# Kernel optimization log

Measured on AMD Instinct MI355X. Metric: run time of the kernel, lower is better.

## Reference

```python
import jax, jax.numpy as jnp
import numpy as np

WIN_SIZE = 9
SIGMA = 1.5
K1, K2 = 0.01, 0.03
ALPHA, BETA = 0.5, 1.0
DATA_RANGE = 2.0
COV_NORM = 1.0  # use_sample_covariance=False


def _gaussian_window():
    coords = jnp.arange(WIN_SIZE, dtype=jnp.float32) - WIN_SIZE // 2
    g = jnp.exp(-coords ** 2 / (2.0 * SIGMA ** 2))
    g = g / g.sum()
    w2d = jnp.outer(g, g)  # [9, 9]
    return w2d[None, None, :, :]  # [1, 1, 9, 9] (OIHW, in_channel=1)


def setup_inputs() -> dict:
    key = jax.random.key(0)
    k1, k2 = jax.random.split(key)
    shape = (32, 1, 1024, 1024)
    X = jax.random.uniform(k1, shape, dtype=jnp.float32) * 2.0 - 1.0
    Y = jax.random.uniform(k2, shape, dtype=jnp.float32) * 2.0 - 1.0
    w = _gaussian_window()
    return {"X": X, "Y": Y, "w": w}


def _dwconv(x, w):
    # depthwise (groups=1 here since in_channel=1), VALID padding (use_pad=False)
    return jax.lax.conv_general_dilated(
        x, w, window_strides=(1, 1), padding="VALID",
        dimension_numbers=("NCHW", "OIHW", "NCHW"), feature_group_count=1)


def reference(X, Y, w):
    C1 = (K1 * DATA_RANGE) ** 2
    C2 = (K2 * DATA_RANGE) ** 2
    ux = _dwconv(X, w)
    uy = _dwconv(Y, w)
    uxx = _dwconv(X * X, w)
    uyy = _dwconv(Y * Y, w)
    uxy = _dwconv(X * Y, w)
    vx = COV_NORM * (uxx - ux * ux)
    vy = COV_NORM * (uyy - uy * uy)
    vxy = COV_NORM * (uxy - ux * uy)
    A1 = 2.0 * ux * uy + C1
    A2 = 2.0 * vxy + C2
    B1 = ux ** 2 + uy ** 2 + C1
    B2 = vx + vy + C2
    S = (A1 * A2) / (B1 * B2)
    ssim_loss = (1.0 - S).mean()
    loss_l1 = jnp.abs(X - Y).mean()
    return ALPHA * ssim_loss + BETA * loss_l1
```

## Files before the change

### kernel.cpp

```cpp
#include <hip/hip_runtime.h>

#define NT 256
#define RROWS 45
#define STRIP 256
#define PW 264
#define NLD 132
#define WID 1024
#define HEI 1024
#define OWD 1016

typedef float v2f __attribute__((ext_vector_type(2)));

template<int I> struct IC { static constexpr int v = I; };
template<int N, int I = 0, typename F>
__device__ __forceinline__ void sfor(F&& f) {
    if constexpr (I < N) { f(IC<I>{}); sfor<N, I + 1>(f); }
}

static __device__ __forceinline__ v2f pkfma(v2f a, v2f b, v2f c) {
#if __has_builtin(__builtin_elementwise_fma)
    return __builtin_elementwise_fma(a, b, c);
#else
    v2f r; r.x = fmaf(a.x, b.x, c.x); r.y = fmaf(a.y, b.y, c.y); return r;
#endif
}

__global__ __launch_bounds__(NT, 2)
void ssim_main(const float* __restrict__ X, const float* __restrict__ Y,
               const float* __restrict__ Wg, double* __restrict__ acc)
{
    __shared__ float2 Prow[9][PW];
    __shared__ float  wsum[4][2];

    const int t  = threadIdx.x;
    const int r0 = blockIdx.x * RROWS;
    const int c0 = blockIdx.y * STRIP;
    const size_t ibase = (size_t)blockIdx.z * (size_t)(WID * HEI);

    const bool ldv  = (t < NLD) && (c0 + 2 * t < WID);
    const bool ownc = (t < 128);

    float g[9];
    {
        float s = 0.f;
        sfor<9>([&](auto K) { constexpr int k = decltype(K)::v;
            g[k] = Wg[36 + k]; s += g[k]; });
        float rs = __builtin_amdgcn_rcpf(s);
        sfor<9>([&](auto K) { constexpr int k = decltype(K)::v; g[k] *= rs; });
    }

    const float C1 = 0.0004f, C2 = 0.0036f;
    float ssim_acc = 0.f, l1_acc = 0.f;

    v2f  r01[9], r23[9];
    float r4[9];
    float2 pbx[3], pby[3];

    const float2* __restrict__ Xp = (const float2*)(X + ibase + c0);
    const float2* __restrict__ Yp = (const float2*)(Y + ibase + c0);

    auto issue = [&](int ro, auto S) {
        constexpr int s = decltype(S)::v;
        const int row = r0 + ro;
        if (ldv && row < HEI) {
            pbx[s] = Xp[(size_t)row * (WID / 2) + t];
            pby[s] = Yp[(size_t)row * (WID / 2) + t];
        }
    };
    auto store = [&](int ro, auto S, auto LS) {
        constexpr int s  = decltype(S)::v;
        constexpr int ls = decltype(LS)::v;
        const int row = r0 + ro;
        if (ldv && row < HEI) {
            float4* dst = (float4*)&Prow[ls][2 * t];
            *dst = make_float4(pbx[s].x, pby[s].x, pbx[s].y, pby[s].y);
            if (ownc && ro < RROWS)
                l1_acc += fabsf(pbx[s].x - pby[s].x) + fabsf(pbx[s].y - pby[s].y);
        }
    };
    auto hcomp = [&](auto LS, auto RS) {
        constexpr int ls = decltype(LS)::v;
        constexpr int rs = decltype(RS)::v;
        v2f s01 = (v2f)0.f, s23 = (v2f)0.f; float s4 = 0.f;
        sfor<9>([&](auto K) { constexpr int k = decltype(K)::v;
            float2 p = Prow[ls][t + k];
            v2f a = { p.x, p.y };
            v2f gk2 = { g[k], g[k] };
            s01 = pkfma(gk2, a, s01);
            s23 = pkfma(gk2, a * a, s23);
            s4  = fmaf(g[k], p.x * p.y, s4);
        });
        r01[rs] = s01; r23[rs] = s23; r4[rs] = s4;
    };

    const bool vA = (c0 + t < OWD);

    auto outrow = [&](int j, auto JM) {
        constexpr int jm = decltype(JM)::v;
        if (r0 + j < OWD) {
            v2f u01 = (v2f)0.f, u23 = (v2f)0.f; float u4 = 0.f;
            sfor<9>([&](auto K) { constexpr int k = decltype(K)::v;
                constexpr int s = (jm + k) % 9;
                v2f gk2 = { g[k], g[k] };
                u01 = pkfma(gk2, r01[s], u01);
                u23 = pkfma(gk2, r23[s], u23);
                u4  = fmaf(g[k], r4[s], u4);
            });
            float ux = u01.x, uy = u01.y, uxx = u23.x, uyy = u23.y, uxy = u4;
            float uxux = ux * ux, uyuy = uy * uy, uxuy = ux * uy;
            float A1 = 2.f * uxuy + C1;
            float A2 = 2.f * (uxy - uxuy) + C2;
            float B1 = uxux + uyuy + C1;
            float B2 = (uxx - uxux) + (uyy - uyuy) + C2;
            float S  = (A1 * A2) * __builtin_amdgcn_rcpf(B1 * B2);
            ssim_acc += vA ? S : 0.f;
        }
    };

    issue(0, IC<0>{}); issue(1, IC<1>{}); issue(2, IC<2>{});
    store(0, IC<0>{}, IC<0>{}); store(1, IC<1>{}, IC<1>{}); store(2, IC<2>{}, IC<2>{});
    __syncthreads();
    issue(3, IC<0>{}); issue(4, IC<1>{}); issue(5, IC<2>{});
    hcomp(IC<0>{}, IC<0>{}); hcomp(IC<1>{}, IC<1>{}); hcomp(IC<2>{}, IC<2>{});

    store(3, IC<0>{}, IC<3>{}); store(4, IC<1>{}, IC<4>{}); store(5, IC<2>{}, IC<5>{});
    __syncthreads();
    issue(6, IC<0>{}); issue(7, IC<1>{}); issue(8, IC<2>{});
    hcomp(IC<3>{}, IC<3>{}); hcomp(IC<4>{}, IC<4>{}); hcomp(IC<5>{}, IC<5>{});

    store(6, IC<0>{}, IC<6>{}); store(7, IC<1>{}, IC<7>{}); store(8, IC<2>{}, IC<8>{});
    __syncthreads();
    issue(9, IC<0>{}); issue(10, IC<1>{}); issue(11, IC<2>{});
    hcomp(IC<6>{}, IC<6>{}); hcomp(IC<7>{}, IC<7>{});

#pragma unroll 1
    for (int P = 0; P < 5; ++P) {
        const int jb = 9 * P;
        sfor<3>([&](auto Q) {
            constexpr int q = decltype(Q)::v;
            const int p  = 3 * P + q;
            const int j0 = jb + 3 * q;
            store(j0 + 9,  IC<0>{}, IC<(3 * q) % 9>{});
            store(j0 + 10, IC<1>{}, IC<(3 * q + 1) % 9>{});
            store(j0 + 11, IC<2>{}, IC<(3 * q + 2) % 9>{});
            __syncthreads();
            if (p < 14) {
                issue(j0 + 12, IC<0>{}); issue(j0 + 13, IC<1>{}); issue(j0 + 14, IC<2>{});
            }
            hcomp(IC<(3 * q + 8) % 9>{}, IC<(3 * q + 8) % 9>{});
            outrow(j0,     IC<(3 * q) % 9>{});
            hcomp(IC<(3 * q + 9) % 9>{}, IC<(3 * q + 9) % 9>{});
            outrow(j0 + 1, IC<(3 * q + 1) % 9>{});
            hcomp(IC<(3 * q + 10) % 9>{}, IC<(3 * q + 10) % 9>{});
            outrow(j0 + 2, IC<(3 * q + 2) % 9>{});
        });
    }

#pragma unroll
    for (int off = 32; off > 0; off >>= 1) {
        ssim_acc += __shfl_down(ssim_acc, off);
        l1_acc   += __shfl_down(l1_acc, off);
    }
    const int wid = t >> 6;
    if ((t & 63) == 0) { wsum[wid][0] = ssim_acc; wsum[wid][1] = l1_acc; }
    __syncthreads();
    if (t == 0) {
        double s = 0.0, l = 0.0;
#pragma unroll
        for (int w = 0; w < 4; ++w) { s += (double)wsum[w][0]; l += (double)wsum[w][1]; }
        atomicAdd(acc + 0, s);
        atomicAdd(acc + 1, l);
    }
}

__global__ void ssim_final(const double* __restrict__ acc, float* __restrict__ out)
{
    const double n_ssim = 33032192.0;
    const double n_l1   = 33554432.0;
    double ssim_loss = 1.0 - acc[0] / n_ssim;
    double l1        = acc[1] / n_l1;
    out[0] = (float)(0.5 * ssim_loss + 1.0 * l1);
}

extern "C" void kernel_launch(void* const* d_in, const int* in_sizes, int n_in,
                              void* d_out, int out_size, void* d_ws, size_t ws_size,
                              hipStream_t stream)
{
    const float* X  = (const float*)d_in[0];
    const float* Y  = (const float*)d_in[1];
    const float* Wg = (const float*)d_in[2];
    float*  out = (float*)d_out;
    double* acc = (double*)d_ws;

    hipMemsetAsync(acc, 0, 2 * sizeof(double), stream);
    dim3 grid(23, 4, 32);
    ssim_main<<<grid, NT, 0, stream>>>(X, Y, Wg, acc);
    ssim_final<<<1, 1, 0, stream>>>(acc, out);
}
```

Measured before the change: 318.6 us.

## Stream rows into LDS ring via direct global_load_lds DMA

Replaces the register-staged loads and interleaved LDS stores with direct global-to-LDS loads (global_load_lds) into a 12-slot ring of separate X and Y row buffers. Synchronisation moves to manual vmcnt waits plus s_barrier, which keeps loads several rows ahead. The L1 term is now read back from LDS instead of registers. The aim is to cut VGPR staging and store instructions and to deepen the prefetch. The risk is fragile vmcnt accounting, tail-row handling and extra LDS space.

```diff
diff --git a/kernel.cpp b/kernel.cpp
--- a/kernel.cpp
+++ b/kernel.cpp
@@ -3,8 +3,8 @@
 #define NT 256
 #define RROWS 45
 #define STRIP 256
-#define PW 264
-#define NLD 132
+#define PWL 264
+#define NRING 12
 #define WID 1024
 #define HEI 1024
 #define OWD 1016
@@ -25,20 +25,48 @@
 #endif
 }
 
+typedef __attribute__((address_space(1))) const void gvoid_t;
+typedef __attribute__((address_space(3))) void svoid_t;
+
+static __device__ __forceinline__ void gld16(const float* gp, float* lp) {
+    __builtin_amdgcn_global_load_lds((gvoid_t*)gp, (svoid_t*)lp, 16, 0, 0);
+}
+
 __global__ __launch_bounds__(NT, 2)
 void ssim_main(const float* __restrict__ X, const float* __restrict__ Y,
                const float* __restrict__ Wg, double* __restrict__ acc)
 {
-    __shared__ float2 Prow[9][PW];
-    __shared__ float  wsum[4][2];
-
-    const int t  = threadIdx.x;
-    const int r0 = blockIdx.x * RROWS;
-    const int c0 = blockIdx.y * STRIP;
+    __shared__ __align__(16) float Xr[NRING][PWL];
+    __shared__ __align__(16) float Yr[NRING][PWL];
+    __shared__ float wsum[4][2];
+
+    const int t    = threadIdx.x;
+    const int wv   = t >> 6, lane = t & 63;
+    const int r0   = blockIdx.x * RROWS;
+    const int c0   = blockIdx.y * STRIP;
     const size_t ibase = (size_t)blockIdx.z * (size_t)(WID * HEI);
 
-    const bool ldv  = (t < NLD) && (c0 + 2 * t < WID);
-    const bool ownc = (t < 128);
+    const float* __restrict__ Xg = X + ibase + c0;
+    const float* __restrict__ Yg = Y + ibase + c0;
+    const int remoff = (c0 + PWL <= WID) ? STRIP : 0;
+
+    auto dma = [&](int ro) {
+        const int row = r0 + ro;
+        if (row >= HEI) return;
+        const int sl = (unsigned)ro % NRING;
+        if (wv == 0)      gld16(Xg + (size_t)row * WID + lane * 4, &Xr[sl][0]);
+        else if (wv == 1) { if (lane < 2) gld16(Xg + (size_t)row * WID + remoff + lane * 4, &Xr[sl][STRIP]); }
+        else if (wv == 2) gld16(Yg + (size_t)row * WID + lane * 4, &Yr[sl][0]);
+        else              { if (lane < 2) gld16(Yg + (size_t)row * WID + remoff + lane * 4, &Yr[sl][STRIP]); }
+    };
+
+    auto wait_barrier = [&](bool drain0, bool w6) {
+        if (drain0)  asm volatile("s_waitcnt vmcnt(0)" ::: "memory");
+        else if (w6) asm volatile("s_waitcnt vmcnt(6)" ::: "memory");
+        else         asm volatile("s_waitcnt vmcnt(3)" ::: "memory");
+        __builtin_amdgcn_s_barrier();
+        asm volatile("" ::: "memory");
+    };
 
     float g[9];
     {
@@ -54,41 +82,27 @@
 
     v2f  r01[9], r23[9];
     float r4[9];
-    float2 pbx[3], pby[3];
-
-    const float2* __restrict__ Xp = (const float2*)(X + ibase + c0);
-    const float2* __restrict__ Yp = (const float2*)(Y + ibase + c0);
-
-    auto issue = [&](int ro, auto S) {
-        constexpr int s = decltype(S)::v;
+
+    auto l1row = [&](int ro) {
         const int row = r0 + ro;
-        if (ldv && row < HEI) {
-            pbx[s] = Xp[(size_t)row * (WID / 2) + t];
-            pby[s] = Yp[(size_t)row * (WID / 2) + t];
+        if (ro < RROWS && row < HEI) {
+            const int sl = (unsigned)ro % NRING;
+            l1_acc += fabsf(Xr[sl][t] - Yr[sl][t]);
         }
     };
-    auto store = [&](int ro, auto S, auto LS) {
-        constexpr int s  = decltype(S)::v;
-        constexpr int ls = decltype(LS)::v;
-        const int row = r0 + ro;
-        if (ldv && row < HEI) {
-            float4* dst = (float4*)&Prow[ls][2 * t];
-            *dst = make_float4(pbx[s].x, pby[s].x, pbx[s].y, pby[s].y);
-            if (ownc && ro < RROWS)
-                l1_acc += fabsf(pbx[s].x - pby[s].x) + fabsf(pbx[s].y - pby[s].y);
-        }
-    };
-    auto hcomp = [&](auto LS, auto RS) {
-        constexpr int ls = decltype(LS)::v;
+
+    auto hcomp = [&](int sl, auto RS) {
         constexpr int rs = decltype(RS)::v;
+        const float* xb = &Xr[sl][t];
+        const float* yb = &Yr[sl][t];
         v2f s01 = (v2f)0.f, s23 = (v2f)0.f; float s4 = 0.f;
         sfor<9>([&](auto K) { constexpr int k = decltype(K)::v;
-            float2 p = Prow[ls][t + k];
-            v2f a = { p.x, p.y };
+            float x = xb[k], y = yb[k];
+            v2f a = { x, y };
             v2f gk2 = { g[k], g[k] };
             s01 = pkfma(gk2, a, s01);
             s23 = pkfma(gk2, a * a, s23);
-            s4  = fmaf(g[k], p.x * p.y, s4);
+            s4  = fmaf(g[k], x * y, s4);
         });
         r01[rs] = s01; r23[rs] = s23; r4[rs] = s4;
     };
@@ -117,41 +131,38 @@
         }
     };
 
-    issue(0, IC<0>{}); issue(1, IC<1>{}); issue(2, IC<2>{});
-    store(0, IC<0>{}, IC<0>{}); store(1, IC<1>{}, IC<1>{}); store(2, IC<2>{}, IC<2>{});
-    __syncthreads();
-    issue(3, IC<0>{}); issue(4, IC<1>{}); issue(5, IC<2>{});
-    hcomp(IC<0>{}, IC<0>{}); hcomp(IC<1>{}, IC<1>{}); hcomp(IC<2>{}, IC<2>{});
-
-    store(3, IC<0>{}, IC<3>{}); store(4, IC<1>{}, IC<4>{}); store(5, IC<2>{}, IC<5>{});
-    __syncthreads();
-    issue(6, IC<0>{}); issue(7, IC<1>{}); issue(8, IC<2>{});
-    hcomp(IC<3>{}, IC<3>{}); hcomp(IC<4>{}, IC<4>{}); hcomp(IC<5>{}, IC<5>{});
-
-    store(6, IC<0>{}, IC<6>{}); store(7, IC<1>{}, IC<7>{}); store(8, IC<2>{}, IC<8>{});
-    __syncthreads();
-    issue(9, IC<0>{}); issue(10, IC<1>{}); issue(11, IC<2>{});
-    hcomp(IC<6>{}, IC<6>{}); hcomp(IC<7>{}, IC<7>{});
+    dma(0); dma(1); dma(2);
+    dma(3); dma(4); dma(5);
+    dma(6); dma(7); dma(8);
+    wait_barrier(false, true);
+    dma(9); dma(10); dma(11);
+    l1row(0); l1row(1); l1row(2);
+    hcomp(0, IC<0>{}); hcomp(1, IC<1>{}); hcomp(2, IC<2>{});
+    wait_barrier(false, true);
+    dma(12); dma(13); dma(14);
+    l1row(3); l1row(4); l1row(5);
+    hcomp(3, IC<3>{}); hcomp(4, IC<4>{}); hcomp(5, IC<5>{});
+    wait_barrier(false, true);
+    l1row(6); l1row(7); l1row(8);
+    hcomp(6, IC<6>{}); hcomp(7, IC<7>{});
+
+    const bool vtail = (r0 + 59 >= HEI);
 
 #pragma unroll 1
     for (int P = 0; P < 5; ++P) {
-        const int jb = 9 * P;
         sfor<3>([&](auto Q) {
             constexpr int q = decltype(Q)::v;
-            const int p  = 3 * P + q;
-            const int j0 = jb + 3 * q;
-            store(j0 + 9,  IC<0>{}, IC<(3 * q) % 9>{});
-            store(j0 + 10, IC<1>{}, IC<(3 * q + 1) % 9>{});
-            store(j0 + 11, IC<2>{}, IC<(3 * q + 2) % 9>{});
-            __syncthreads();
-            if (p < 14) {
-                issue(j0 + 12, IC<0>{}); issue(j0 + 13, IC<1>{}); issue(j0 + 14, IC<2>{});
-            }
-            hcomp(IC<(3 * q + 8) % 9>{}, IC<(3 * q + 8) % 9>{});
+            const int p   = 3 * P + q;
+            const int j0  = 3 * p;
+            const int ro8 = j0 + 8;
+            wait_barrier(vtail || p == 14, false);
+            if (p <= 12) { dma(j0 + 15); dma(j0 + 16); dma(j0 + 17); }
+            l1row(j0 + 9); l1row(j0 + 10); l1row(j0 + 11);
+            hcomp((unsigned)(ro8)     % NRING, IC<(3 * q + 8) % 9>{});
             outrow(j0,     IC<(3 * q) % 9>{});
-            hcomp(IC<(3 * q + 9) % 9>{}, IC<(3 * q + 9) % 9>{});
+            hcomp((unsigned)(ro8 + 1) % NRING, IC<(3 * q + 9) % 9>{});
             outrow(j0 + 1, IC<(3 * q + 1) % 9>{});
-            hcomp(IC<(3 * q + 10) % 9>{}, IC<(3 * q + 10) % 9>{});
+            hcomp((unsigned)(ro8 + 2) % NRING, IC<(3 * q + 10) % 9>{});
             outrow(j0 + 2, IC<(3 * q + 2) % 9>{});
         });
     }
```

Result: slower. 342.6 us (+7.5%).
